# Kernel optimization log

Measured on AMD Instinct MI355X. Metric: run time of the kernel, lower is better.

## Reference

```python
import jax, jax.numpy as jnp
import numpy as np

BN_EPS = 1e-5


def setup_inputs() -> dict:
    key = jax.random.key(0)
    ks = jax.random.split(key, 12)
    B, T, S = 8, 256, 64
    D = 256  # 2*u, u=128
    sc = lambda fan: 1.0 / np.sqrt(fan)
    return {
        "Hx": jax.random.normal(ks[0], (B, T, D), dtype=jnp.float32),
        "Hs": jax.random.normal(ks[1], (S, D), dtype=jnp.float32),
        # transformS = BatchNorm1d(D) -> Linear(D,D) -> ReLU -> Linear(D,D)
        "bn_gamma": jnp.ones((D,), jnp.float32),
        "bn_beta": jnp.zeros((D,), jnp.float32),
        "s_w1": jax.random.normal(ks[2], (D, D), jnp.float32) * sc(D),
        "s_b1": jnp.zeros((D,), jnp.float32),
        "s_w2": jax.random.normal(ks[3], (D, D), jnp.float32) * sc(D),
        "s_b2": jnp.zeros((D,), jnp.float32),
        # W = Linear(3D, D) -> ReLU -> Linear(D, 1)   (6u = 3D features)
        "w_w1": jax.random.normal(ks[4], (3 * D, D), jnp.float32) * sc(3 * D),
        "w_b1": jnp.zeros((D,), jnp.float32),
        "w_w2": jax.random.normal(ks[5], (D, 1), jnp.float32) * sc(D),
        "w_b2": jnp.zeros((1,), jnp.float32),
        "truthSeqY": jax.random.randint(ks[6], (B, T, S), 0, 2, dtype=jnp.int32),
        "inputLen": jax.random.randint(ks[7], (B,), 1, T, dtype=jnp.int32),
    }


def reference(Hx, Hs, bn_gamma, bn_beta, s_w1, s_b1, s_w2, s_b2,
              w_w1, w_b1, w_w2, w_b2, truthSeqY, inputLen):
    B, T, D = Hx.shape
    S = Hs.shape[0]

    # transformS: BatchNorm1d (training-mode batch stats over slot dim) + 2-layer MLP
    mu = jnp.mean(Hs, axis=0)
    var = jnp.var(Hs, axis=0)  # biased, as torch BN uses for normalization
    hs = (Hs - mu) * jax.lax.rsqrt(var + BN_EPS) * bn_gamma + bn_beta
    transHs = jax.nn.relu(hs @ s_w1 + s_b1) @ s_w2 + s_b2  # [S, D]

    # pairwise broadcast: cat(Hx, transHs, Hx*transHs) over [B,T,S,3D]
    mx = jnp.broadcast_to(Hx[:, :, None, :], (B, T, S, D))
    ms = jnp.broadcast_to(transHs[None, None, :, :], (B, T, S, D))
    feat = jnp.concatenate([mx, ms, mx * ms], axis=-1)  # [B,T,S,3D]

    # scoring MLP -> scalar per (token, slot)
    h = jax.nn.relu(feat @ w_w1 + w_b1)        # [B,T,S,D]
    atten = (h @ w_w2 + w_b2)[..., 0]          # [B,T,S]

    atten_score = jax.nn.softmax(atten, axis=2)             # softmax over slots
    G = jnp.einsum('bts,sd->btd', atten_score, transHs)     # weighted slot agg
    outputU = jnp.concatenate([Hx, G + Hx], axis=2)         # [B,T,2D]
    return outputU, atten_score
```

## Files before the change

kernel.cpp:

```cpp
#include <hip/hip_runtime.h>
#include <math.h>

#define DD 256
#define SS 64
#define BT 2048

typedef __attribute__((ext_vector_type(4))) float f32x4;
typedef __attribute__((ext_vector_type(8))) short bf16x8;
typedef __attribute__((ext_vector_type(4))) unsigned int u32x4;

typedef __attribute__((address_space(3))) unsigned lds_u32;
typedef const __attribute__((address_space(1))) unsigned glb_u32;

__device__ inline unsigned pack_bf16(float a, float b) {
    unsigned ua = __builtin_bit_cast(unsigned, a);
    unsigned ub = __builtin_bit_cast(unsigned, b);
    ua = (ua + 0x7fffu + ((ua >> 16) & 1u)) >> 16;
    ub = (ub + 0x7fffu + ((ub >> 16) & 1u)) >> 16;
    return ua | (ub << 16);
}

__global__ __launch_bounds__(1024) void
k_prep2(const float* __restrict__ Hs, const float* __restrict__ g,
        const float* __restrict__ b, const float* __restrict__ s_w1,
        const float* __restrict__ s_b1, const float* __restrict__ s_w2,
        const float* __restrict__ s_b2, const float* __restrict__ w_w1,
        const float* __restrict__ w_b1, float* __restrict__ transHs,
        float* __restrict__ S1b) {
    __shared__ float rowA[DD], rowB[DD], rowC[DD];
    __shared__ float red[8][DD];
    const int s = blockIdx.x;
    const int j = threadIdx.x & 255, kw = threadIdx.x >> 8;
    float sum = 0.f, sumsq = 0.f;
#pragma unroll
    for (int s2 = kw * 16; s2 < kw * 16 + 16; ++s2) {
        float v = Hs[s2 * DD + j];
        sum += v; sumsq += v * v;
    }
    red[kw][j] = sum; red[4 + kw][j] = sumsq;
    __syncthreads();
    if (kw == 0) {
        float st = red[0][j] + red[1][j] + red[2][j] + red[3][j];
        float sq = red[4][j] + red[5][j] + red[6][j] + red[7][j];
        float mu  = st * (1.f / SS);
        float var = sq * (1.f / SS) - mu * mu;
        rowA[j] = (Hs[s * DD + j] - mu) * rsqrtf(var + 1e-5f) * g[j] + b[j];
    }
    __syncthreads();
    float a1 = 0.f;
#pragma unroll 16
    for (int d = kw * 64; d < kw * 64 + 64; ++d)
        a1 = fmaf(rowA[d], s_w1[d * DD + j], a1);
    red[kw][j] = a1;
    __syncthreads();
    if (kw == 0)
        rowB[j] = fmaxf(red[0][j] + red[1][j] + red[2][j] + red[3][j] + s_b1[j], 0.f);
    __syncthreads();
    float a2 = 0.f;
#pragma unroll 16
    for (int d = kw * 64; d < kw * 64 + 64; ++d)
        a2 = fmaf(rowB[d], s_w2[d * DD + j], a2);
    red[kw][j] = a2;
    __syncthreads();
    if (kw == 0) {
        float r = red[0][j] + red[1][j] + red[2][j] + red[3][j] + s_b2[j];
        rowC[j] = r;
        transHs[s * DD + j] = r;
    }
    __syncthreads();
    float a3 = 0.f;
#pragma unroll 16
    for (int d = kw * 64; d < kw * 64 + 64; ++d)
        a3 = fmaf(rowC[d], w_w1[(256 + d) * DD + j], a3);
    red[kw][j] = a3;
    __syncthreads();
    if (kw == 0)
        S1b[s * DD + j] = red[0][j] + red[1][j] + red[2][j] + red[3][j] + w_b1[j];
}

__global__ __launch_bounds__(256) void
k_pack(const float* __restrict__ Hx, const float* __restrict__ w_w1,
       const float* __restrict__ transHs, unsigned* __restrict__ Apack,
       unsigned* __restrict__ Bs) {
    const int bid = blockIdx.x;
    const int tid = threadIdx.x;
    if (bid < 256) {
        int idx = bid * 256 + tid;
        int lane = idx & 63, ks = (idx >> 6) & 7, MT = idx >> 9;
        int t  = MT * 16 + (lane & 15);
        int k0 = ks * 32 + (lane >> 4) * 8;
        const float* src = Hx + t * DD + k0;
        float4 x0 = *(const float4*)src;
        float4 x1 = *(const float4*)(src + 4);
        unsigned p[4];
        p[0] = pack_bf16(x0.x, x0.y);
        p[1] = pack_bf16(x0.z, x0.w);
        p[2] = pack_bf16(x1.x, x1.y);
        p[3] = pack_bf16(x1.z, x1.w);
        *(u32x4*)(Apack + idx * 4) = *(const u32x4*)p;
    } else {
        __shared__ float ms_l[16][DD];
        const int b2 = bid - 256;
        const int ic = b2 & 31, sg = b2 >> 5;
        const int s0 = sg * 16;
#pragma unroll
        for (int i = 0; i < 4; ++i) {
            int e4 = i * 256 + tid;
            ((float4*)ms_l)[e4] = ((const float4*)(transHs + s0 * DD))[e4];
        }
        __syncthreads();
        const int idx = ic * 256 + tid;
        const int lane = idx & 63, ks = (idx >> 6) & 7, nt = idx >> 9;
        const int j  = nt * 16 + (lane & 15);
        const int k0 = ks * 32 + (lane >> 4) * 8;
        const float* C = w_w1 + 512 * DD;
        float w1v[8], cv[8];
#pragma unroll
        for (int e = 0; e < 8; ++e) {
            w1v[e] = w_w1[(k0 + e) * DD + j];
            cv[e]  = C[(k0 + e) * DD + j];
        }
        for (int ss = 0; ss < 16; ++ss) {
            unsigned p[4];
#pragma unroll
            for (int e = 0; e < 4; ++e) {
                float f0 = w1v[2 * e]     + ms_l[ss][k0 + 2 * e]     * cv[2 * e];
                float f1 = w1v[2 * e + 1] + ms_l[ss][k0 + 2 * e + 1] * cv[2 * e + 1];
                p[e] = pack_bf16(f0, f1);
            }
            *(u32x4*)(Bs + ((s0 + ss) * 8192 + idx) * 4) = *(const u32x4*)p;
        }
    }
}

__global__ __launch_bounds__(512, 4) void
k_main_mfma(const unsigned* __restrict__ Apack, const unsigned* __restrict__ Bs,
            const float* __restrict__ S1b, const float* __restrict__ w2,
            const float* __restrict__ w_b2, float* __restrict__ atten) {
    __shared__ unsigned Albs[16384];
    __shared__ float attp[8][128];
    const int bid = blockIdx.x;
    const int xcd = bid & 7, li = bid >> 3;
    const int sp  = xcd * 4 + (li >> 4);
    const int tile = li & 15;
    const int t0 = tile * 128;
    const int tid = threadIdx.x;
    const int w = tid >> 6, l = tid & 63;
    const int lrow = l & 15, lg = l >> 4;
    const unsigned* Asrc = Apack + tile * 16384;

#pragma unroll
    for (int i = 0; i < 8; ++i) {
        int chunk = w * 8 + i;
        __builtin_amdgcn_global_load_lds((glb_u32*)(Asrc + chunk * 256 + l * 4),
                                         (lds_u32*)(Albs + chunk * 256), 16, 0, 0);
    }
    __syncthreads();

    const float w2v0 = w2[(w * 2 + 0) * 16 + lrow];
    const float w2v1 = w2[(w * 2 + 1) * 16 + lrow];

    for (int sl = 0; sl < 2; ++sl) {
        const int s = sp * 2 + sl;
        const unsigned* Bsl = Bs + s * 32768;
        f32x4 acc[8][2] = {};
#pragma unroll
        for (int ks = 0; ks < 8; ++ks) {
            bf16x8 af[8];
#pragma unroll
            for (int mt = 0; mt < 8; ++mt)
                af[mt] = *(const bf16x8*)((const char*)Albs + ((mt * 8 + ks) * 64 + l) * 16);
#pragma unroll
            for (int nt = 0; nt < 2; ++nt) {
                const bf16x8 bf = *(const bf16x8*)(Bsl + (((w * 2 + nt) * 8 + ks) * 64 + l) * 4);
#pragma unroll
                for (int mt = 0; mt < 8; ++mt)
                    acc[mt][nt] = __builtin_amdgcn_mfma_f32_16x16x32_bf16(af[mt], bf, acc[mt][nt], 0, 0, 0);
            }
        }
        const float s10 = S1b[s * DD + (w * 2 + 0) * 16 + lrow];
        const float s11 = S1b[s * DD + (w * 2 + 1) * 16 + lrow];
#pragma unroll
        for (int mt = 0; mt < 8; ++mt) {
#pragma unroll
            for (int i = 0; i < 4; ++i) {
                float p = fmaxf(acc[mt][0][i] + s10, 0.f) * w2v0
                        + fmaxf(acc[mt][1][i] + s11, 0.f) * w2v1;
                p += __shfl_xor(p, 1);
                p += __shfl_xor(p, 2);
                p += __shfl_xor(p, 4);
                p += __shfl_xor(p, 8);
                if (lrow == 0) attp[w][mt * 16 + lg * 4 + i] = p;
            }
        }
        __syncthreads();
        if (tid < 128) {
            float r = attp[0][tid] + attp[1][tid] + attp[2][tid] + attp[3][tid]
                    + attp[4][tid] + attp[5][tid] + attp[6][tid] + attp[7][tid] + w_b2[0];
            atten[(t0 + tid) * SS + s] = r;
        }
        __syncthreads();
    }
}

__global__ __launch_bounds__(256) void
k_out(const float* __restrict__ Hx, const float* __restrict__ m,
      const float* __restrict__ atten, float* __restrict__ outU,
      float* __restrict__ outA) {
    int wave = threadIdx.x >> 6, lane = threadIdx.x & 63;
    int t = blockIdx.x * 4 + wave;
    float a = atten[t * SS + lane];
    float mx = a;
#pragma unroll
    for (int off = 32; off; off >>= 1) mx = fmaxf(mx, __shfl_xor(mx, off));
    float e = __expf(a - mx);
    float sum = e;
#pragma unroll
    for (int off = 32; off; off >>= 1) sum += __shfl_xor(sum, off);
    float p = e / sum;
    outA[t * SS + lane] = p;
    float gacc[4] = {};
    for (int s = 0; s < SS; ++s) {
        float ps = __shfl(p, s);
#pragma unroll
        for (int q = 0; q < 4; ++q)
            gacc[q] = fmaf(ps, m[s * DD + lane + 64 * q], gacc[q]);
    }
#pragma unroll
    for (int q = 0; q < 4; ++q) {
        int j = lane + 64 * q;
        float x = Hx[t * DD + j];
        outU[t * 2 * DD + j] = x;
        outU[t * 2 * DD + DD + j] = x + gacc[q];
    }
}

extern "C" void kernel_launch(void* const* d_in, const int* in_sizes, int n_in,
                              void* d_out, int out_size, void* d_ws, size_t ws_size,
                              hipStream_t stream) {
    const float* Hx   = (const float*)d_in[0];
    const float* Hs   = (const float*)d_in[1];
    const float* bn_g = (const float*)d_in[2];
    const float* bn_b = (const float*)d_in[3];
    const float* s_w1 = (const float*)d_in[4];
    const float* s_b1 = (const float*)d_in[5];
    const float* s_w2 = (const float*)d_in[6];
    const float* s_b2 = (const float*)d_in[7];
    const float* w_w1 = (const float*)d_in[8];
    const float* w_b1 = (const float*)d_in[9];
    const float* w_w2 = (const float*)d_in[10];
    const float* w_b2 = (const float*)d_in[11];

    float* ws      = (float*)d_ws;
    float* transHs = ws;
    float* S1b     = ws + 16384;
    float* atten   = ws + 32768;
    unsigned* Apack = (unsigned*)(ws + 163840);
    unsigned* Bs    = Apack + 262144;

    float* outU = (float*)d_out;
    float* outA = outU + BT * 2 * DD;

    k_prep2<<<SS, 1024, 0, stream>>>(Hs, bn_g, bn_b, s_w1, s_b1, s_w2, s_b2,
                                     w_w1, w_b1, transHs, S1b);
    k_pack<<<384, 256, 0, stream>>>(Hx, w_w1, transHs, Apack, Bs);
    k_main_mfma<<<512, 512, 0, stream>>>(Apack, Bs, S1b, w_w2, w_b2, atten);
    k_out<<<BT / 4, 256, 0, stream>>>(Hx, transHs, atten, outU, outA);
}
```

Measured before the change: 63.57 us.

## Fuse four kernels into one cooperative persistent kernel with grid syncs

```diff
diff --git a/kernel.cpp b/kernel.cpp
--- a/kernel.cpp
+++ b/kernel.cpp
@@ -1,5 +1,8 @@
 #include <hip/hip_runtime.h>
+#include <hip/hip_cooperative_groups.h>
 #include <math.h>
+
+namespace cg = cooperative_groups;
 
 #define DD 256
 #define SS 64
@@ -18,6 +21,210 @@
     ua = (ua + 0x7fffu + ((ua >> 16) & 1u)) >> 16;
     ub = (ub + 0x7fffu + ((ub >> 16) & 1u)) >> 16;
     return ua | (ub << 16);
+}
+
+__global__ __launch_bounds__(512, 2) void
+k_fused(const float* Hx, const float* Hs, const float* bn_g, const float* bn_b,
+        const float* s_w1, const float* s_b1, const float* s_w2, const float* s_b2,
+        const float* w_w1, const float* w_b1, const float* w_w2, const float* w_b2,
+        float* transHs, float* S1b, float* atten,
+        unsigned* Apack, unsigned* Bs, float* outU, float* outA) {
+    __shared__ unsigned Albs[16384];
+    __shared__ float attp[8][128];
+    float* F = (float*)Albs;
+    const int bid = blockIdx.x;
+    const int tid = threadIdx.x;
+    const int w = tid >> 6, l = tid & 63;
+    cg::grid_group grid = cg::this_grid();
+
+    if (bid < 64) {
+        const int s = bid, j = tid & 255, kw = tid >> 8;
+        float* rowA = F; float* rowB = F + 256; float* rowC = F + 512;
+        float* red  = F + 768;
+        float sum = 0.f, sumsq = 0.f;
+#pragma unroll
+        for (int s2 = kw * 32; s2 < kw * 32 + 32; ++s2) {
+            float v = Hs[s2 * DD + j];
+            sum += v; sumsq += v * v;
+        }
+        red[kw * 256 + j] = sum; red[512 + kw * 256 + j] = sumsq;
+        __syncthreads();
+        if (kw == 0) {
+            float st = red[j] + red[256 + j];
+            float sq = red[512 + j] + red[768 + j];
+            float mu  = st * (1.f / SS);
+            float var = sq * (1.f / SS) - mu * mu;
+            rowA[j] = (Hs[s * DD + j] - mu) * rsqrtf(var + 1e-5f) * bn_g[j] + bn_b[j];
+        }
+        __syncthreads();
+        float a1 = 0.f;
+#pragma unroll 8
+        for (int d = kw * 128; d < kw * 128 + 128; ++d)
+            a1 = fmaf(rowA[d], s_w1[d * DD + j], a1);
+        red[kw * 256 + j] = a1;
+        __syncthreads();
+        if (kw == 0) rowB[j] = fmaxf(red[j] + red[256 + j] + s_b1[j], 0.f);
+        __syncthreads();
+        float a2 = 0.f;
+#pragma unroll 8
+        for (int d = kw * 128; d < kw * 128 + 128; ++d)
+            a2 = fmaf(rowB[d], s_w2[d * DD + j], a2);
+        red[kw * 256 + j] = a2;
+        __syncthreads();
+        if (kw == 0) {
+            float r = red[j] + red[256 + j] + s_b2[j];
+            rowC[j] = r;
+            transHs[s * DD + j] = r;
+        }
+        __syncthreads();
+        float a3 = 0.f;
+#pragma unroll 8
+        for (int d = kw * 128; d < kw * 128 + 128; ++d)
+            a3 = fmaf(rowC[d], w_w1[(256 + d) * DD + j], a3);
+        red[kw * 256 + j] = a3;
+        __syncthreads();
+        if (kw == 0) S1b[s * DD + j] = red[j] + red[256 + j] + w_b1[j];
+    } else {
+        int gidx = (bid - 64) * 512 + tid;
+        if (gidx < 65536) {
+            int lane = gidx & 63, ks = (gidx >> 6) & 7, MT = gidx >> 9;
+            int t  = MT * 16 + (lane & 15);
+            int k0 = ks * 32 + (lane >> 4) * 8;
+            const float* src = Hx + t * DD + k0;
+            float4 x0 = *(const float4*)src;
+            float4 x1 = *(const float4*)(src + 4);
+            unsigned p[4];
+            p[0] = pack_bf16(x0.x, x0.y);
+            p[1] = pack_bf16(x0.z, x0.w);
+            p[2] = pack_bf16(x1.x, x1.y);
+            p[3] = pack_bf16(x1.z, x1.w);
+            *(u32x4*)(Apack + gidx * 4) = *(const u32x4*)p;
+        }
+    }
+    grid.sync();
+
+    {
+        const int sg = bid >> 5, ic = bid & 31;
+        const int s0 = sg * 8;
+        ((float4*)F)[tid] = ((const float4*)(transHs + s0 * DD))[tid];
+        __syncthreads();
+        const int idxl = tid & 255, half = tid >> 8;
+        const int idx  = ic * 256 + idxl;
+        const int lane = idx & 63, ks = (idx >> 6) & 7, nt = idx >> 9;
+        const int j  = nt * 16 + (lane & 15);
+        const int k0 = ks * 32 + (lane >> 4) * 8;
+        const float* C = w_w1 + 512 * DD;
+        float w1v[8], cv[8];
+#pragma unroll
+        for (int e = 0; e < 8; ++e) {
+            w1v[e] = w_w1[(k0 + e) * DD + j];
+            cv[e]  = C[(k0 + e) * DD + j];
+        }
+#pragma unroll
+        for (int ss2 = 0; ss2 < 4; ++ss2) {
+            const int ss = half * 4 + ss2;
+            const float* msr = F + ss * 256;
+            unsigned p[4];
+#pragma unroll
+            for (int e = 0; e < 4; ++e) {
+                float f0 = w1v[2 * e]     + msr[k0 + 2 * e]     * cv[2 * e];
+                float f1 = w1v[2 * e + 1] + msr[k0 + 2 * e + 1] * cv[2 * e + 1];
+                p[e] = pack_bf16(f0, f1);
+            }
+            *(u32x4*)(Bs + ((s0 + ss) * 8192 + idx) * 4) = *(const u32x4*)p;
+        }
+    }
+    grid.sync();
+
+    {
+        const int xcd = bid & 7, li = bid >> 3;
+        const int sq  = xcd * 2 + (li >> 4);
+        const int tile = li & 15;
+        const int t0 = tile * 128;
+        const int lrow = l & 15, lg = l >> 4;
+        const unsigned* Asrc = Apack + tile * 16384;
+#pragma unroll
+        for (int i = 0; i < 8; ++i) {
+            int chunk = w * 8 + i;
+            __builtin_amdgcn_global_load_lds((glb_u32*)(Asrc + chunk * 256 + l * 4),
+                                             (lds_u32*)(Albs + chunk * 256), 16, 0, 0);
+        }
+        __syncthreads();
+
+        const float w2v0 = w_w2[(w * 2 + 0) * 16 + lrow];
+        const float w2v1 = w_w2[(w * 2 + 1) * 16 + lrow];
+
+        for (int sl = 0; sl < 4; ++sl) {
+            const int s = sq * 4 + sl;
+            const unsigned* Bsl = Bs + s * 32768;
+            f32x4 acc[8][2] = {};
+#pragma unroll
+            for (int ks = 0; ks < 8; ++ks) {
+                bf16x8 af[8];
+#pragma unroll
+                for (int mt = 0; mt < 8; ++mt)
+                    af[mt] = *(const bf16x8*)((const char*)Albs + ((mt * 8 + ks) * 64 + l) * 16);
+#pragma unroll
+                for (int nt = 0; nt < 2; ++nt) {
+                    const bf16x8 bf = *(const bf16x8*)(Bsl + (((w * 2 + nt) * 8 + ks) * 64 + l) * 4);
+#pragma unroll
+                    for (int mt = 0; mt < 8; ++mt)
+                        acc[mt][nt] = __builtin_amdgcn_mfma_f32_16x16x32_bf16(af[mt], bf, acc[mt][nt], 0, 0, 0);
+                }
+            }
+            const float s10 = S1b[s * DD + (w * 2 + 0) * 16 + lrow];
+            const float s11 = S1b[s * DD + (w * 2 + 1) * 16 + lrow];
+#pragma unroll
+            for (int mt = 0; mt < 8; ++mt) {
+#pragma unroll
+                for (int i = 0; i < 4; ++i) {
+                    float p = fmaxf(acc[mt][0][i] + s10, 0.f) * w2v0
+                            + fmaxf(acc[mt][1][i] + s11, 0.f) * w2v1;
+                    p += __shfl_xor(p, 1);
+                    p += __shfl_xor(p, 2);
+                    p += __shfl_xor(p, 4);
+                    p += __shfl_xor(p, 8);
+                    if (lrow == 0) attp[w][mt * 16 + lg * 4 + i] = p;
+                }
+            }
+            __syncthreads();
+            if (tid < 128) {
+                float r = attp[0][tid] + attp[1][tid] + attp[2][tid] + attp[3][tid]
+                        + attp[4][tid] + attp[5][tid] + attp[6][tid] + attp[7][tid] + w_b2[0];
+                atten[(t0 + tid) * SS + s] = r;
+            }
+            __syncthreads();
+        }
+    }
+    grid.sync();
+
+    {
+        int t = bid * 8 + w;
+        float a = atten[t * SS + l];
+        float mx = a;
+#pragma unroll
+        for (int off = 32; off; off >>= 1) mx = fmaxf(mx, __shfl_xor(mx, off));
+        float e = __expf(a - mx);
+        float sum = e;
+#pragma unroll
+        for (int off = 32; off; off >>= 1) sum += __shfl_xor(sum, off);
+        float p = e / sum;
+        outA[t * SS + l] = p;
+        float gacc[4] = {};
+        for (int s = 0; s < SS; ++s) {
+            float ps = __shfl(p, s);
+#pragma unroll
+            for (int q = 0; q < 4; ++q)
+                gacc[q] = fmaf(ps, transHs[s * DD + l + 64 * q], gacc[q]);
+        }
+#pragma unroll
+        for (int q = 0; q < 4; ++q) {
+            int j = l + 64 * q;
+            float x = Hx[t * DD + j];
+            outU[t * 2 * DD + j] = x;
+            outU[t * 2 * DD + DD + j] = x + gacc[q];
+        }
+    }
 }
 
 __global__ __launch_bounds__(1024) void
@@ -148,7 +355,6 @@
     const int w = tid >> 6, l = tid & 63;
     const int lrow = l & 15, lg = l >> 4;
     const unsigned* Asrc = Apack + tile * 16384;
-
 #pragma unroll
     for (int i = 0; i < 8; ++i) {
         int chunk = w * 8 + i;
@@ -156,10 +362,8 @@
                                          (lds_u32*)(Albs + chunk * 256), 16, 0, 0);
     }
     __syncthreads();
-
     const float w2v0 = w2[(w * 2 + 0) * 16 + lrow];
     const float w2v1 = w2[(w * 2 + 1) * 16 + lrow];
-
     for (int sl = 0; sl < 2; ++sl) {
         const int s = sp * 2 + sl;
         const unsigned* Bsl = Bs + s * 32768;
@@ -261,9 +465,18 @@
     float* outU = (float*)d_out;
     float* outA = outU + BT * 2 * DD;
 
-    k_prep2<<<SS, 1024, 0, stream>>>(Hs, bn_g, bn_b, s_w1, s_b1, s_w2, s_b2,
-                                     w_w1, w_b1, transHs, S1b);
-    k_pack<<<384, 256, 0, stream>>>(Hx, w_w1, transHs, Apack, Bs);
-    k_main_mfma<<<512, 512, 0, stream>>>(Apack, Bs, S1b, w_w2, w_b2, atten);
-    k_out<<<BT / 4, 256, 0, stream>>>(Hx, transHs, atten, outU, outA);
-}
+    void* args[] = {(void*)&Hx, (void*)&Hs, (void*)&bn_g, (void*)&bn_b,
+                    (void*)&s_w1, (void*)&s_b1, (void*)&s_w2, (void*)&s_b2,
+                    (void*)&w_w1, (void*)&w_b1, (void*)&w_w2, (void*)&w_b2,
+                    (void*)&transHs, (void*)&S1b, (void*)&atten,
+                    (void*)&Apack, (void*)&Bs, (void*)&outU, (void*)&outA};
+    hipError_t err = hipLaunchCooperativeKernel((void*)k_fused, dim3(256), dim3(512),
+                                                args, 0, stream);
+    if (err != hipSuccess) {
+        k_prep2<<<SS, 1024, 0, stream>>>(Hs, bn_g, bn_b, s_w1, s_b1, s_w2, s_b2,
+                                         w_w1, w_b1, transHs, S1b);
+        k_pack<<<384, 256, 0, stream>>>(Hx, w_w1, transHs, Apack, Bs);
+        k_main_mfma<<<512, 512, 0, stream>>>(Apack, Bs, S1b, w_w2, w_b2, atten);
+        k_out<<<BT / 4, 256, 0, stream>>>(Hx, transHs, atten, outU, outA);
+    }
+}
```

Result: slower. 173.6 us (+173.1%).
